# Kernel tuning notes

Hardware: AMD Instinct MI355X
Metric: run time of the kernel (lower is better)

Reference implementation:

```python
import jax, jax.numpy as jnp
import numpy as np

N = 100000   # nodes
E = 1600000  # edges
H = 256      # hidden_channels
C_IN = 1
C_OUT = 6
B = 64       # graphs in batch


def setup_inputs() -> dict:
    key = jax.random.key(0)
    ks = jax.random.split(key, 14)
    x = jax.random.normal(ks[0], (N, C_IN), jnp.float32)
    edge_index = jax.random.randint(ks[1], (2, E), 0, N, dtype=jnp.int64)
    batch = jnp.sort(jax.random.randint(ks[2], (N,), 0, B, dtype=jnp.int64))
    svm_pred = jax.random.uniform(ks[3], (B,), jnp.float32)

    def w(k, shape, fan_in):
        return jax.random.normal(k, shape, jnp.float32) * (1.0 / np.sqrt(fan_in))

    return {
        "x": x, "edge_index": edge_index, "batch": batch, "svm_pred": svm_pred,
        "W1": w(ks[4], (C_IN, H), C_IN),  "b1": jnp.zeros((H,), jnp.float32),
        "W2": w(ks[5], (H, H), H),        "b2": jnp.zeros((H,), jnp.float32),
        "W3": w(ks[6], (H, H), H),        "b3": jnp.zeros((H,), jnp.float32),
        "Wf1": w(ks[7], (H + 1, 128), H + 1), "bf1": jnp.zeros((128,), jnp.float32),
        "Wf2": w(ks[8], (128, C_OUT), 128),   "bf2": jnp.zeros((C_OUT,), jnp.float32),
    }


def reference(x, edge_index, batch, svm_pred,
              W1, b1, W2, b2, W3, b3, Wf1, bf1, Wf2, bf2):
    # --- GCN normalization (PyG GCNConv default: add self-loops, sym norm) ---
    loops = jnp.arange(N, dtype=edge_index.dtype)
    src = jnp.concatenate([edge_index[0], loops])  # [E+N]
    dst = jnp.concatenate([edge_index[1], loops])  # [E+N]
    deg = jax.ops.segment_sum(jnp.ones_like(dst, dtype=x.dtype), dst, num_segments=N)
    dinv = deg ** -0.5  # deg >= 1 due to self-loops
    norm = dinv[src] * dinv[dst]  # [E+N]

    def gcn(h, W, b):
        hw = h @ W                                   # [N, H]
        msg = hw[src] * norm[:, None]                # gather + scale
        return jax.ops.segment_sum(msg, dst, num_segments=N) + b

    # Dropout is identity in eval mode.
    h = jax.nn.relu(gcn(x, W1, b1))
    h = jax.nn.relu(gcn(h, W2, b2))
    h = jax.nn.relu(gcn(h, W3, b3))

    # global_mean_pool over graph ids
    sums = jax.ops.segment_sum(h, batch, num_segments=B)            # [B, H]
    cnts = jax.ops.segment_sum(jnp.ones((N,), h.dtype), batch, num_segments=B)
    pooled = sums / jnp.maximum(cnts, 1.0)[:, None]

    feat = jnp.concatenate([pooled, svm_pred.reshape(-1, 1).astype(h.dtype)], axis=1)
    out = jax.nn.relu(feat @ Wf1 + bf1) @ Wf2 + bf2                 # [B, 6]
    return out
```

## Files before the change

kernel.cpp:

```cpp
#include <hip/hip_runtime.h>
#include <math.h>

#define N_NODES 100000
#define N_EDGES 1600000
#define HDIM    256
#define NGRAPH  64

#define SCAN_BLK 1024
#define SCAN_NB  ((N_NODES + SCAN_BLK - 1) / SCAN_BLK)

#define FB 128

typedef __attribute__((ext_vector_type(8))) short bf16x8;
typedef __attribute__((ext_vector_type(4))) float f32x4;
typedef __attribute__((ext_vector_type(8))) unsigned short u16x8;

__device__ __forceinline__ ushort f2b(float f) {
    union { float f; unsigned u; } x; x.f = f;
    unsigned u = x.u;
    unsigned r = u + 0x7fffu + ((u >> 16) & 1u);
    return (ushort)(r >> 16);
}
__device__ __forceinline__ float b2f(ushort h) {
    union { unsigned u; float f; } x; x.u = ((unsigned)h) << 16;
    return x.f;
}

__global__ void k_count(const int* __restrict__ ei, int* __restrict__ cnt,
                        int* __restrict__ slot) {
    int t = blockIdx.x * blockDim.x + threadIdx.x;
    int e0 = t * 8;
    if (e0 >= N_EDGES) return;
    int d[8];
#pragma unroll
    for (int j = 0; j < 8; ++j) d[j] = ei[N_EDGES + e0 + j];
    int s[8];
#pragma unroll
    for (int j = 0; j < 8; ++j) s[j] = atomicAdd(&cnt[d[j]], 1);
#pragma unroll
    for (int j = 0; j < 8; ++j) slot[e0 + j] = s[j];
}

__global__ __launch_bounds__(1024) void k_scan1(const int* __restrict__ cnt,
                                                int* __restrict__ rowptr,
                                                int* __restrict__ bsum) {
    __shared__ int lds[SCAN_BLK];
    int t = threadIdx.x;
    int i = blockIdx.x * SCAN_BLK + t;
    int v = (i < N_NODES) ? cnt[i] : 0;
    lds[t] = v;
    __syncthreads();
    for (int off = 1; off < SCAN_BLK; off <<= 1) {
        int u = (t >= off) ? lds[t - off] : 0;
        __syncthreads();
        lds[t] += u;
        __syncthreads();
    }
    if (i < N_NODES) rowptr[i] = lds[t] - v;
    if (t == SCAN_BLK - 1) bsum[blockIdx.x] = lds[t];
}

__global__ __launch_bounds__(128) void k_scan2(int* __restrict__ bsum) {
    __shared__ int lds[128];
    int t = threadIdx.x;
    int v = (t < SCAN_NB) ? bsum[t] : 0;
    lds[t] = v;
    __syncthreads();
    for (int off = 1; off < 128; off <<= 1) {
        int u = (t >= off) ? lds[t - off] : 0;
        __syncthreads();
        lds[t] += u;
        __syncthreads();
    }
    if (t < SCAN_NB) bsum[t] = lds[t] - v;
}

__global__ void k_dinv_fix(const int* __restrict__ cnt, const float* __restrict__ x,
                           const int* __restrict__ bsum,
                           float* __restrict__ dinv, float* __restrict__ xd,
                           int* __restrict__ rowptr) {
    int i = blockIdx.x * blockDim.x + threadIdx.x;
    if (i < N_NODES) {
        rowptr[i] += bsum[i >> 10];
        float d = (float)(cnt[i] + 1);
        float dv = 1.0f / sqrtf(d);
        dinv[i] = dv;
        xd[i] = x[i] * dv;
        if (i == 0) rowptr[N_NODES] = N_EDGES;
    }
}

__global__ void k_fill(const int* __restrict__ ei, const int* __restrict__ rowptr,
                       const int* __restrict__ slot, int* __restrict__ colv) {
    int t = blockIdx.x * blockDim.x + threadIdx.x;
    int e0 = t * 4;
    if (e0 >= N_EDGES) return;
    int d[4], sl[4], sr[4];
#pragma unroll
    for (int j = 0; j < 4; ++j) {
        d[j] = ei[N_EDGES + e0 + j];
        sl[j] = slot[e0 + j];
        sr[j] = ei[e0 + j];
    }
    int rp[4];
#pragma unroll
    for (int j = 0; j < 4; ++j) rp[j] = rowptr[d[j]];
#pragma unroll
    for (int j = 0; j < 4; ++j) colv[rp[j] + sl[j]] = sr[j];
}

__global__ __launch_bounds__(256) void k_s(const int* __restrict__ rowptr,
                                           const int* __restrict__ colv,
                                           const float* __restrict__ xd,
                                           const float* __restrict__ dinv,
                                           float2* __restrict__ sd) {
    int wid = threadIdx.x >> 6, lane = threadIdx.x & 63;
    int node = blockIdx.x * 4 + wid;
    if (node >= N_NODES) return;
    int s = rowptr[node], e = rowptr[node + 1];
    float acc = 0.f;
    for (int idx = s + lane; idx < e; idx += 64) acc += xd[colv[idx]];
#pragma unroll
    for (int off = 32; off; off >>= 1) acc += __shfl_xor(acc, off);
    if (lane == 0) {
        float dv = dinv[node];
        sd[node] = make_float2(dv * (acc + xd[node]), dv);
    }
}

__global__ __launch_bounds__(256) void k_packW2(const float* __restrict__ Wa,
                                                ushort* __restrict__ Wpa,
                                                const float* __restrict__ Wb,
                                                ushort* __restrict__ Wpb) {
    int bid = blockIdx.x;
    const float* W = (bid < 32) ? Wa : Wb;
    ushort* Wp = (bid < 32) ? Wpa : Wpb;
    int t = (bid & 31) * 256 + threadIdx.x;
    int lane = t & 63;
    int nt = (t >> 6) & 15;
    int k0 = t >> 10;
    int col = nt * 16 + (lane & 15);
    int kb = k0 * 32 + (lane >> 4) * 8;
    ushort o[8];
#pragma unroll
    for (int j = 0; j < 8; ++j) o[j] = f2b(W[(size_t)(kb + j) * HDIM + col]);
    *(ushort4*)&Wp[(size_t)t * 8 + 0] = make_ushort4(o[0], o[1], o[2], o[3]);
    *(ushort4*)&Wp[(size_t)t * 8 + 4] = make_ushort4(o[4], o[5], o[6], o[7]);
}

__global__ __launch_bounds__(512, 4) void k_fused23(
    const int* __restrict__ rowptr, const int* __restrict__ colv,
    const float2* __restrict__ sd,
    const float* __restrict__ W1, const float* __restrict__ b1,
    const ushort* __restrict__ Wp2, const float* __restrict__ b2,
    const ushort* __restrict__ Wp3, const float* __restrict__ dinv,
    ushort* __restrict__ C) {
    __shared__ __align__(16) ushort lds[FB * 256];
    char* ldsb = (char*)lds;
    int tid = threadIdx.x;
    int wave = tid >> 6, lane = tid & 63;
    int blk0 = blockIdx.x * FB;

    {
        int c4 = lane * 4;
        float4 w = *(const float4*)&W1[c4];
        float4 b = *(const float4*)&b1[c4];
        for (int i = 0; i < 16; ++i) {
            int l = wave * 16 + i;
            int node = blk0 + l;
            if (node >= N_NODES) break;
            float2 self = sd[node];
            float a0 = self.y * fmaxf(fmaf(self.x, w.x, b.x), 0.f);
            float a1 = self.y * fmaxf(fmaf(self.x, w.y, b.y), 0.f);
            float a2 = self.y * fmaxf(fmaf(self.x, w.z, b.z), 0.f);
            float a3 = self.y * fmaxf(fmaf(self.x, w.w, b.w), 0.f);
            int s0 = rowptr[node], e0 = rowptr[node + 1];
            for (int base = s0; base < e0; base += 64) {
                int idx = base + lane;
                float2 p = make_float2(0.f, 0.f);
                if (idx < e0) p = sd[colv[idx]];
                int rem = min(64, e0 - base);
                for (int k = 0; k < rem; ++k) {
                    float ps = __shfl(p.x, k);
                    float pd = __shfl(p.y, k);
                    a0 += pd * fmaxf(fmaf(ps, w.x, b.x), 0.f);
                    a1 += pd * fmaxf(fmaf(ps, w.y, b.y), 0.f);
                    a2 += pd * fmaxf(fmaf(ps, w.z, b.z), 0.f);
                    a3 += pd * fmaxf(fmaf(ps, w.w, b.w), 0.f);
                }
            }
            float dvi = self.y;
            uint2 pk;
            pk.x = (unsigned)f2b(a0 * dvi) | ((unsigned)f2b(a1 * dvi) << 16);
            pk.y = (unsigned)f2b(a2 * dvi) | ((unsigned)f2b(a3 * dvi) << 16);
            unsigned off = (unsigned)l * 512 + (((unsigned)lane * 8) ^ (((unsigned)(l & 7)) << 4));
            *(uint2*)(ldsb + off) = pk;
        }
    }
    __syncthreads();

    int l = wave * 16 + (lane & 15);
    int node = blk0 + l;
    int kgrp = lane >> 4;
    bool ok = node < N_NODES;
    unsigned swz = ((unsigned)(l & 7)) << 4;
    unsigned rowb = (unsigned)l * 512;

    f32x4 acc[16];
#pragma unroll
    for (int nt = 0; nt < 16; ++nt) acc[nt] = (f32x4){0.f, 0.f, 0.f, 0.f};
#pragma unroll 1
    for (int k0 = 0; k0 < 8; ++k0) {
        bf16x8 bf = *(const bf16x8*)(ldsb + rowb + (((unsigned)(16 * kgrp + 64 * k0)) ^ swz));
        const ushort* wp = Wp2 + ((size_t)k0 * 1024 + lane) * 8;
#pragma unroll
        for (int nt = 0; nt < 16; ++nt) {
            bf16x8 a = *(const bf16x8*)(wp + (size_t)nt * 512);
            acc[nt] = __builtin_amdgcn_mfma_f32_16x16x32_bf16(a, bf, acc[nt], 0, 0, 0);
        }
    }
    __syncthreads();

#pragma unroll
    for (int nt = 0; nt < 16; ++nt) {
        int f = nt * 16 + kgrp * 4;
        float4 bv = *(const float4*)&b2[f];
        uint2 pk;
        pk.x = (unsigned)f2b(fmaxf(acc[nt][0] + bv.x, 0.f)) |
               ((unsigned)f2b(fmaxf(acc[nt][1] + bv.y, 0.f)) << 16);
        pk.y = (unsigned)f2b(fmaxf(acc[nt][2] + bv.z, 0.f)) |
               ((unsigned)f2b(fmaxf(acc[nt][3] + bv.w, 0.f)) << 16);
        *(uint2*)(ldsb + rowb + (((unsigned)(f * 2)) ^ swz)) = pk;
    }
    __syncthreads();

#pragma unroll
    for (int nt = 0; nt < 16; ++nt) acc[nt] = (f32x4){0.f, 0.f, 0.f, 0.f};
#pragma unroll 1
    for (int k0 = 0; k0 < 8; ++k0) {
        bf16x8 bf = *(const bf16x8*)(ldsb + rowb + (((unsigned)(16 * kgrp + 64 * k0)) ^ swz));
        const ushort* wp = Wp3 + ((size_t)k0 * 1024 + lane) * 8;
#pragma unroll
        for (int nt = 0; nt < 16; ++nt) {
            bf16x8 a = *(const bf16x8*)(wp + (size_t)nt * 512);
            acc[nt] = __builtin_amdgcn_mfma_f32_16x16x32_bf16(a, bf, acc[nt], 0, 0, 0);
        }
    }
    if (ok) {
        float dv = dinv[node];
        size_t base = (size_t)node * HDIM + kgrp * 4;
#pragma unroll
        for (int nt = 0; nt < 16; ++nt) {
            ushort4 o;
            o.x = f2b(acc[nt][0] * dv);
            o.y = f2b(acc[nt][1] * dv);
            o.z = f2b(acc[nt][2] * dv);
            o.w = f2b(acc[nt][3] * dv);
            *(ushort4*)&C[base + nt * 16] = o;
        }
    }
}

__global__ __launch_bounds__(256) void k_agg(const ushort* __restrict__ g,
                                             const int* __restrict__ rowptr,
                                             const int* __restrict__ colv,
                                             const float* __restrict__ dinv,
                                             const float* __restrict__ bias,
                                             ushort* __restrict__ hout) {
    int wid = threadIdx.x >> 6, lane = threadIdx.x & 63;
    int node = blockIdx.x * 4 + wid;
    if (node >= N_NODES) return;
    int half = lane >> 5;
    int l32 = lane & 31;
    int c8 = l32 * 8;
    float acc[8];
    if (half == 0) {
        u16x8 v = *(const u16x8*)&g[(size_t)node * HDIM + c8];
#pragma unroll
        for (int j = 0; j < 8; ++j) acc[j] = b2f(v[j]);
    } else {
#pragma unroll
        for (int j = 0; j < 8; ++j) acc[j] = 0.f;
    }
    int s = rowptr[node], e = rowptr[node + 1];
    int i = s;
    for (; i + 8 <= e; i += 8) {
        int base = i + half * 4;
        int n0 = colv[base + 0];
        int n1 = colv[base + 1];
        int n2 = colv[base + 2];
        int n3 = colv[base + 3];
        u16x8 v0 = *(const u16x8*)&g[(size_t)n0 * HDIM + c8];
        u16x8 v1 = *(const u16x8*)&g[(size_t)n1 * HDIM + c8];
        u16x8 v2 = *(const u16x8*)&g[(size_t)n2 * HDIM + c8];
        u16x8 v3 = *(const u16x8*)&g[(size_t)n3 * HDIM + c8];
#pragma unroll
        for (int j = 0; j < 8; ++j)
            acc[j] += (b2f(v0[j]) + b2f(v1[j])) + (b2f(v2[j]) + b2f(v3[j]));
    }
    if (i + 4 <= e) {
        int base = i + half * 2;
        int n0 = colv[base + 0];
        int n1 = colv[base + 1];
        u16x8 v0 = *(const u16x8*)&g[(size_t)n0 * HDIM + c8];
        u16x8 v1 = *(const u16x8*)&g[(size_t)n1 * HDIM + c8];
#pragma unroll
        for (int j = 0; j < 8; ++j) acc[j] += b2f(v0[j]) + b2f(v1[j]);
        i += 4;
    }
    if (i + 2 <= e) {
        int n = colv[i + half];
        u16x8 v = *(const u16x8*)&g[(size_t)n * HDIM + c8];
#pragma unroll
        for (int j = 0; j < 8; ++j) acc[j] += b2f(v[j]);
        i += 2;
    }
    if (i < e && half == 0) {
        int n = colv[i];
        u16x8 v = *(const u16x8*)&g[(size_t)n * HDIM + c8];
#pragma unroll
        for (int j = 0; j < 8; ++j) acc[j] += b2f(v[j]);
    }
#pragma unroll
    for (int j = 0; j < 8; ++j) acc[j] += __shfl_xor(acc[j], 32);
    if (half == 0) {
        float dv = dinv[node];
        float4 bl = *(const float4*)&bias[c8];
        float4 bh = *(const float4*)&bias[c8 + 4];
        float bj[8] = {bl.x, bl.y, bl.z, bl.w, bh.x, bh.y, bh.z, bh.w};
        u16x8 ov;
#pragma unroll
        for (int j = 0; j < 8; ++j)
            ov[j] = f2b(fmaxf(fmaf(acc[j], dv, bj[j]), 0.f));
        *(u16x8*)&hout[(size_t)node * HDIM + c8] = ov;
    }
}

__global__ __launch_bounds__(128) void k_bounds(const int* __restrict__ batch,
                                                int* __restrict__ startb,
                                                float* __restrict__ pooled) {
    int t = threadIdx.x;
    if (t <= NGRAPH) {
        int lo = 0, hi = N_NODES;
        while (lo < hi) {
            int mid = (lo + hi) >> 1;
            if (batch[mid] < t) lo = mid + 1; else hi = mid;
        }
        startb[t] = lo;
    }
    for (int i = t; i < NGRAPH * HDIM; i += 128) pooled[i] = 0.f;
}

__global__ __launch_bounds__(256) void k_pool(const ushort* __restrict__ h,
                                              const int* __restrict__ startb,
                                              float* __restrict__ pooled) {
    int b = blockIdx.x >> 3, c = blockIdx.x & 7;
    int s0 = startb[b], e0 = startb[b + 1];
    int len = e0 - s0;
    if (len <= 0) return;
    int per = (len + 7) >> 3;
    int is = s0 + c * per;
    int ie = min(is + per, e0);
    if (is >= ie) return;
    int j = threadIdx.x;
    float sum = 0.f;
    for (int n = is; n < ie; ++n) sum += b2f(h[(size_t)n * HDIM + j]);
    atomicAdd(&pooled[b * HDIM + j], sum);
}

__global__ __launch_bounds__(128) void k_mlp(const float* __restrict__ pooled,
                                             const int* __restrict__ startb,
                                             const float* __restrict__ svm,
                                             const float* __restrict__ Wf1,
                                             const float* __restrict__ bf1,
                                             const float* __restrict__ Wf2,
                                             const float* __restrict__ bf2,
                                             float* __restrict__ out) {
    __shared__ float fl[257];
    __shared__ float hl[128];
    int b = blockIdx.x;
    int j = threadIdx.x;
    float cntb = fmaxf((float)(startb[b + 1] - startb[b]), 1.0f);
    for (int k = j; k < 256; k += 128) fl[k] = pooled[b * HDIM + k] / cntb;
    if (j == 0) fl[256] = svm[b];
    __syncthreads();
    float acc = bf1[j];
    for (int k = 0; k < 257; ++k) acc = fmaf(fl[k], Wf1[k * 128 + j], acc);
    hl[j] = fmaxf(acc, 0.f);
    __syncthreads();
    if (j < 6) {
        float o = bf2[j];
        for (int k = 0; k < 128; ++k) o = fmaf(hl[k], Wf2[k * 6 + j], o);
        out[b * 6 + j] = o;
    }
}

static inline size_t al256(size_t x) { return (x + 255) & ~(size_t)255; }

extern "C" void kernel_launch(void* const* d_in, const int* in_sizes, int n_in,
                              void* d_out, int out_size, void* d_ws, size_t ws_size,
                              hipStream_t stream) {
    const float* x    = (const float*)d_in[0];
    const int*   ei   = (const int*)d_in[1];
    const int*   batch= (const int*)d_in[2];
    const float* svm  = (const float*)d_in[3];
    const float* W1   = (const float*)d_in[4];
    const float* b1   = (const float*)d_in[5];
    const float* W2   = (const float*)d_in[6];
    const float* b2   = (const float*)d_in[7];
    const float* W3   = (const float*)d_in[8];
    const float* b3   = (const float*)d_in[9];
    const float* Wf1  = (const float*)d_in[10];
    const float* bf1  = (const float*)d_in[11];
    const float* Wf2  = (const float*)d_in[12];
    const float* bf2  = (const float*)d_in[13];
    float* out = (float*)d_out;

    char* w = (char*)d_ws;
    int*    cnt    = (int*)w;    w += al256((size_t)N_NODES * 4);
    int*    rowptr = (int*)w;    w += al256((size_t)(N_NODES + 1) * 4);
    int*    slot   = (int*)w;    w += al256((size_t)N_EDGES * 4);
    int*    colv   = (int*)w;    w += al256((size_t)N_EDGES * 4);
    float*  dinv   = (float*)w;  w += al256((size_t)N_NODES * 4);
    float*  xd     = (float*)w;  w += al256((size_t)N_NODES * 4);
    float2* sd     = (float2*)w; w += al256((size_t)N_NODES * 8);
    int*    startb = (int*)w;    w += al256(65 * 4);
    int*    bsum   = (int*)w;    w += al256((size_t)SCAN_NB * 4);
    float*  pooled = (float*)w;  w += al256((size_t)NGRAPH * HDIM * 4);
    ushort* Wp2    = (ushort*)w; w += al256((size_t)8 * 16 * 64 * 8 * 2);
    ushort* Wp3    = (ushort*)w; w += al256((size_t)8 * 16 * 64 * 8 * 2);
    ushort* bigA   = (ushort*)w; w += al256((size_t)N_NODES * HDIM * 2);
    ushort* bigB   = (ushort*)w; w += al256((size_t)N_NODES * HDIM * 2);

    const int nblkN = (N_NODES + 255) / 256;
    const int nblkW = (N_NODES + 3) / 4;
    const int nblkF = (N_NODES + FB - 1) / FB;

    hipMemsetAsync(cnt, 0, (size_t)N_NODES * 4, stream);
    k_count<<<(N_EDGES / 8 + 255) / 256, 256, 0, stream>>>(ei, cnt, slot);
    k_scan1<<<SCAN_NB, SCAN_BLK, 0, stream>>>(cnt, rowptr, bsum);
    k_scan2<<<1, 128, 0, stream>>>(bsum);
    k_dinv_fix<<<nblkN, 256, 0, stream>>>(cnt, x, bsum, dinv, xd, rowptr);
    k_fill<<<(N_EDGES / 4 + 255) / 256, 256, 0, stream>>>(ei, rowptr, slot, colv);

    k_packW2<<<64, 256, 0, stream>>>(W2, Wp2, W3, Wp3);

    k_s<<<nblkW, 256, 0, stream>>>(rowptr, colv, xd, dinv, sd);

    k_fused23<<<nblkF, 512, 0, stream>>>(rowptr, colv, sd, W1, b1,
                                         Wp2, b2, Wp3, dinv, bigB);

    k_agg<<<nblkW, 256, 0, stream>>>(bigB, rowptr, colv, dinv, b3, bigA);

    k_bounds<<<1, 128, 0, stream>>>(batch, startb, pooled);
    k_pool<<<NGRAPH * 8, 256, 0, stream>>>(bigA, startb, pooled);
    k_mlp<<<NGRAPH, 128, 0, stream>>>(pooled, startb, svm, Wf1, bf1, Wf2, bf2, out);
}
```

Before: 488.7 us.

## Split layer-2 aggregation out of fused GEMM kernel into separate pass

Moves the per-node layer-1 activation and neighbor aggregation out of the fused GEMM kernel into its own one-wave-per-node kernel that writes a bf16 intermediate to global memory, with the shuffle loop unrolled by four. The GEMM kernel now reads its operand from global memory instead of LDS, runs with 256 threads and 64-row tiles, and drops a barrier. This is meant to fix load imbalance from the irregular aggregation inside the large fused block and to raise occupancy of the MFMA stage. The cost is an extra round trip of a 51 MB intermediate through global memory and one more kernel launch.

```diff
diff --git a/kernel.cpp b/kernel.cpp
--- a/kernel.cpp
+++ b/kernel.cpp
@@ -9,7 +9,7 @@
 #define SCAN_BLK 1024
 #define SCAN_NB  ((N_NODES + SCAN_BLK - 1) / SCAN_BLK)
 
-#define FB 128
+#define FB 64
 
 typedef __attribute__((ext_vector_type(8))) short bf16x8;
 typedef __attribute__((ext_vector_type(4))) float f32x4;
@@ -128,6 +128,70 @@
     }
 }
 
+__global__ __launch_bounds__(256) void k_aggM(const int* __restrict__ rowptr,
+                                              const int* __restrict__ colv,
+                                              const float2* __restrict__ sd,
+                                              const float* __restrict__ W1,
+                                              const float* __restrict__ b1,
+                                              ushort* __restrict__ M) {
+    int wid = threadIdx.x >> 6, lane = threadIdx.x & 63;
+    int node = blockIdx.x * 4 + wid;
+    if (node >= N_NODES) return;
+    int c4 = lane * 4;
+    float4 w = *(const float4*)&W1[c4];
+    float4 b = *(const float4*)&b1[c4];
+    float2 self = sd[node];
+    float a0 = self.y * fmaxf(fmaf(self.x, w.x, b.x), 0.f);
+    float a1 = self.y * fmaxf(fmaf(self.x, w.y, b.y), 0.f);
+    float a2 = self.y * fmaxf(fmaf(self.x, w.z, b.z), 0.f);
+    float a3 = self.y * fmaxf(fmaf(self.x, w.w, b.w), 0.f);
+    int s = rowptr[node], e = rowptr[node + 1];
+    for (int base = s; base < e; base += 64) {
+        int idx = base + lane;
+        float2 p = make_float2(0.f, 0.f);
+        if (idx < e) p = sd[colv[idx]];
+        int rem = min(64, e - base);
+        int k = 0;
+        for (; k + 4 <= rem; k += 4) {
+            float ps0 = __shfl(p.x, k),     pd0 = __shfl(p.y, k);
+            float ps1 = __shfl(p.x, k + 1), pd1 = __shfl(p.y, k + 1);
+            float ps2 = __shfl(p.x, k + 2), pd2 = __shfl(p.y, k + 2);
+            float ps3 = __shfl(p.x, k + 3), pd3 = __shfl(p.y, k + 3);
+            a0 += pd0 * fmaxf(fmaf(ps0, w.x, b.x), 0.f)
+                + pd1 * fmaxf(fmaf(ps1, w.x, b.x), 0.f)
+                + pd2 * fmaxf(fmaf(ps2, w.x, b.x), 0.f)
+                + pd3 * fmaxf(fmaf(ps3, w.x, b.x), 0.f);
+            a1 += pd0 * fmaxf(fmaf(ps0, w.y, b.y), 0.f)
+                + pd1 * fmaxf(fmaf(ps1, w.y, b.y), 0.f)
+                + pd2 * fmaxf(fmaf(ps2, w.y, b.y), 0.f)
+                + pd3 * fmaxf(fmaf(ps3, w.y, b.y), 0.f);
+            a2 += pd0 * fmaxf(fmaf(ps0, w.z, b.z), 0.f)
+                + pd1 * fmaxf(fmaf(ps1, w.z, b.z), 0.f)
+                + pd2 * fmaxf(fmaf(ps2, w.z, b.z), 0.f)
+                + pd3 * fmaxf(fmaf(ps3, w.z, b.z), 0.f);
+            a3 += pd0 * fmaxf(fmaf(ps0, w.w, b.w), 0.f)
+                + pd1 * fmaxf(fmaf(ps1, w.w, b.w), 0.f)
+                + pd2 * fmaxf(fmaf(ps2, w.w, b.w), 0.f)
+                + pd3 * fmaxf(fmaf(ps3, w.w, b.w), 0.f);
+        }
+        for (; k < rem; ++k) {
+            float ps = __shfl(p.x, k);
+            float pd = __shfl(p.y, k);
+            a0 += pd * fmaxf(fmaf(ps, w.x, b.x), 0.f);
+            a1 += pd * fmaxf(fmaf(ps, w.y, b.y), 0.f);
+            a2 += pd * fmaxf(fmaf(ps, w.z, b.z), 0.f);
+            a3 += pd * fmaxf(fmaf(ps, w.w, b.w), 0.f);
+        }
+    }
+    float dvi = self.y;
+    ushort4 o;
+    o.x = f2b(a0 * dvi);
+    o.y = f2b(a1 * dvi);
+    o.z = f2b(a2 * dvi);
+    o.w = f2b(a3 * dvi);
+    *(ushort4*)&M[(size_t)node * HDIM + c4] = o;
+}
+
 __global__ __launch_bounds__(256) void k_packW2(const float* __restrict__ Wa,
                                                 ushort* __restrict__ Wpa,
                                                 const float* __restrict__ Wb,
@@ -148,10 +212,8 @@
     *(ushort4*)&Wp[(size_t)t * 8 + 4] = make_ushort4(o[4], o[5], o[6], o[7]);
 }
 
-__global__ __launch_bounds__(512, 4) void k_fused23(
-    const int* __restrict__ rowptr, const int* __restrict__ colv,
-    const float2* __restrict__ sd,
-    const float* __restrict__ W1, const float* __restrict__ b1,
+__global__ __launch_bounds__(256) void k_g23(
+    const ushort* __restrict__ M,
     const ushort* __restrict__ Wp2, const float* __restrict__ b2,
     const ushort* __restrict__ Wp3, const float* __restrict__ dinv,
     ushort* __restrict__ C) {
@@ -159,48 +221,8 @@
     char* ldsb = (char*)lds;
     int tid = threadIdx.x;
     int wave = tid >> 6, lane = tid & 63;
-    int blk0 = blockIdx.x * FB;
-
-    {
-        int c4 = lane * 4;
-        float4 w = *(const float4*)&W1[c4];
-        float4 b = *(const float4*)&b1[c4];
-        for (int i = 0; i < 16; ++i) {
-            int l = wave * 16 + i;
-            int node = blk0 + l;
-            if (node >= N_NODES) break;
-            float2 self = sd[node];
-            float a0 = self.y * fmaxf(fmaf(self.x, w.x, b.x), 0.f);
-            float a1 = self.y * fmaxf(fmaf(self.x, w.y, b.y), 0.f);
-            float a2 = self.y * fmaxf(fmaf(self.x, w.z, b.z), 0.f);
-            float a3 = self.y * fmaxf(fmaf(self.x, w.w, b.w), 0.f);
-            int s0 = rowptr[node], e0 = rowptr[node + 1];
-            for (int base = s0; base < e0; base += 64) {
-                int idx = base + lane;
-                float2 p = make_float2(0.f, 0.f);
-                if (idx < e0) p = sd[colv[idx]];
-                int rem = min(64, e0 - base);
-                for (int k = 0; k < rem; ++k) {
-                    float ps = __shfl(p.x, k);
-                    float pd = __shfl(p.y, k);
-                    a0 += pd * fmaxf(fmaf(ps, w.x, b.x), 0.f);
-                    a1 += pd * fmaxf(fmaf(ps, w.y, b.y), 0.f);
-                    a2 += pd * fmaxf(fmaf(ps, w.z, b.z), 0.f);
-                    a3 += pd * fmaxf(fmaf(ps, w.w, b.w), 0.f);
-                }
-            }
-            float dvi = self.y;
-            uint2 pk;
-            pk.x = (unsigned)f2b(a0 * dvi) | ((unsigned)f2b(a1 * dvi) << 16);
-            pk.y = (unsigned)f2b(a2 * dvi) | ((unsigned)f2b(a3 * dvi) << 16);
-            unsigned off = (unsigned)l * 512 + (((unsigned)lane * 8) ^ (((unsigned)(l & 7)) << 4));
-            *(uint2*)(ldsb + off) = pk;
-        }
-    }
-    __syncthreads();
-
     int l = wave * 16 + (lane & 15);
-    int node = blk0 + l;
+    int node = blockIdx.x * FB + l;
     int kgrp = lane >> 4;
     bool ok = node < N_NODES;
     unsigned swz = ((unsigned)(l & 7)) << 4;
@@ -209,9 +231,11 @@
     f32x4 acc[16];
 #pragma unroll
     for (int nt = 0; nt < 16; ++nt) acc[nt] = (f32x4){0.f, 0.f, 0.f, 0.f};
+    const ushort* ap = M + (size_t)(ok ? node : 0) * HDIM + kgrp * 8;
 #pragma unroll 1
     for (int k0 = 0; k0 < 8; ++k0) {
-        bf16x8 bf = *(const bf16x8*)(ldsb + rowb + (((unsigned)(16 * kgrp + 64 * k0)) ^ swz));
+        bf16x8 bf = *(const bf16x8*)(ap + k0 * 32);
+        if (!ok) bf = (bf16x8){0, 0, 0, 0, 0, 0, 0, 0};
         const ushort* wp = Wp2 + ((size_t)k0 * 1024 + lane) * 8;
 #pragma unroll
         for (int nt = 0; nt < 16; ++nt) {
@@ -219,7 +243,6 @@
             acc[nt] = __builtin_amdgcn_mfma_f32_16x16x32_bf16(a, bf, acc[nt], 0, 0, 0);
         }
     }
-    __syncthreads();
 
 #pragma unroll
     for (int nt = 0; nt < 16; ++nt) {
@@ -447,8 +470,9 @@
 
     k_s<<<nblkW, 256, 0, stream>>>(rowptr, colv, xd, dinv, sd);
 
-    k_fused23<<<nblkF, 512, 0, stream>>>(rowptr, colv, sd, W1, b1,
-                                         Wp2, b2, Wp3, dinv, bigB);
+    k_aggM<<<nblkW, 256, 0, stream>>>(rowptr, colv, sd, W1, b1, bigA);
+
+    k_g23<<<nblkF, 256, 0, stream>>>(bigA, Wp2, b2, Wp3, dinv, bigB);
 
     k_agg<<<nblkW, 256, 0, stream>>>(bigB, rowptr, colv, dinv, b3, bigA);
 
```

Result: faster. 466.7 us (-4.5%).
